# Performance work log

Measured on AMD Instinct MI355X. Metric: run time of the kernel, lower is better.

The kernel has to match this reference:

```python
import jax, jax.numpy as jnp
import numpy as np

OUT, IN, SPEC = 4096, 4096, 512


def _boundprop(last_uA, weight, bias, preact_lb, preact_ub, alpha):
    # simplex_coefficient: relu(W + b[:,None]) - relu(b[:,None]), shape [OUT, IN]
    simplex_coeff = jax.nn.relu(weight + bias[:, None]) - jax.nn.relu(bias[:, None])
    pos_uA = jnp.maximum(last_uA, 0.0)  # [1, SPEC, OUT]
    neg_uA = jnpum if False else jnp.minimum(last_uA, 0.0)

    # ---- simplex branch ----
    lb_u = preact_lb[..., None]  # [1, OUT, 1]
    ub_u = preact_ub[..., None]
    upper_coeff = jnp.where(ub_u <= 0, 0.0, jnp.where(lb_u >= 0, weight, simplex_coeff))  # [1,OUT,IN]
    upper_bias = jnp.where(preact_ub <= 0, 0.0,
                           jnp.where(preact_lb >= 0, bias, jnp.maximum(bias, 0.0)))  # [1,OUT]
    lower_d = (jnp.abs(preact_lb) >= jnp.abs(preact_ub)).astype(last_uA.dtype)  # [1,OUT]
    lower_coeff = jnp.where(ub_u <= 0, 0.0,
                            jnp.where(lb_u >= 0, weight, lower_d[..., None] * weight))  # [1,OUT,IN]
    lower_bias = jnp.where(preact_ub <= 0, 0.0,
                           jnp.where(preact_lb >= 0, bias, lower_d * bias))  # [1,OUT]
    one_minus_a = 1.0 - alpha              # [1,OUT,1]
    one_minus_a_s = 1.0 - alpha[..., 0]    # [1,OUT]
    upper_coeff = one_minus_a * upper_coeff
    lower_coeff = one_minus_a * lower_coeff
    upper_bias = one_minus_a_s * upper_bias
    lower_bias = one_minus_a_s * lower_bias
    simplex_uA = (jnp.einsum('bso,boi->bsi', pos_uA, upper_coeff)
                  + jnp.einsum('bso,boi->bsi', neg_uA, lower_coeff))  # [1,SPEC,IN]
    simplex_ubias = (jnp.einsum('bso,o->bs', pos_uA, upper_bias[0])
                     + jnp.einsum('bso,o->bs', neg_uA, lower_bias[0]))  # [1,SPEC]

    # ---- crown branch ----
    lb_r = jnp.minimum(preact_lb, 0.0)
    ub_r = jnp.maximum(preact_ub, 0.0)
    ub_r = jnp.maximum(ub_r, lb_r + 1e-8)
    upper_d = ub_r / (ub_r - lb_r)  # [1,OUT]
    upper_b = -lb_r * upper_d       # [1,OUT]
    ud = upper_d[:, None, :]        # [1,1,OUT]
    ld = (ud > 0.5).astype(last_uA.dtype)
    crown_uA_pre = ud * pos_uA + ld * neg_uA  # [1,SPEC,OUT]
    crown_ubias = jnp.einsum('bso,bo->bs', pos_uA, upper_b)  # [1,SPEC]
    w = alpha * weight              # [1,OUT,IN]
    b = alpha[..., 0] * bias        # [1,OUT]
    crown_uA = jnp.einsum('bso,boi->bsi', crown_uA_pre, w)   # [1,SPEC,IN]
    crown_ubias = crown_ubias + jnp.einsum('bso,o->bs', crown_uA_pre, b[0])

    return simplex_uA + crown_uA, simplex_ubias + crown_ubias


def setup_inputs() -> dict:
    key = jax.random.key(0)
    k1, k2, k3, k4, k5 = jax.random.split(key, 5)
    weight = jax.random.normal(k1, (OUT, IN), jnp.float32) * 0.02
    bias = jax.random.normal(k2, (OUT,), jnp.float32) * 0.02
    preact_lb = jax.random.normal(k3, (1, OUT), jnp.float32)
    # ensure ub > lb, with mixed-sign ranges so all relaxation branches are hit
    preact_ub = preact_lb + jnp.abs(jax.random.normal(k4, (1, OUT), jnp.float32)) + 1e-2
    last_uA = jax.random.normal(k5, (1, SPEC, OUT), jnp.float32)
    alpha = jnp.ones((1, OUT, 1), jnp.float32)
    return {'last_uA': last_uA, 'weight': weight, 'bias': bias,
            'preact_lb': preact_lb, 'preact_ub': preact_ub, 'alpha': alpha}


def reference(last_uA, weight, bias, preact_lb, preact_ub, alpha):
    uA, ubias = _boundprop(last_uA, weight, bias, preact_lb, preact_ub, alpha)
    return uA, ubias
```

## Files before the change

kernel.cpp:

```cpp
#include <hip/hip_runtime.h>
#include <hip/hip_bf16.h>
#include <stdint.h>

#define OUTN 4096
#define INN  4096
#define SPECN 512
#define BK 128
#define KT (OUTN / BK)

typedef __attribute__((ext_vector_type(8))) short short8;
typedef __attribute__((ext_vector_type(4))) float f32x4;

__device__ __forceinline__ ushort f2bf(float f) {
    uint32_t u = __float_as_uint(f);
    uint32_t r = (u + 0x7FFFu + ((u >> 16) & 1u)) >> 16;
    return (ushort)r;
}
__device__ __forceinline__ float bf2f(ushort u) {
    return __uint_as_float((uint32_t)u << 16);
}

__global__ __launch_bounds__(256) void prep(
    const float* __restrict__ uA, const float* __restrict__ W,
    const float* __restrict__ Bias, const float* __restrict__ Lb,
    const float* __restrict__ Ub, const float* __restrict__ Alpha,
    ushort* __restrict__ A1, ushort* __restrict__ A2, ushort* __restrict__ WT,
    unsigned long long* __restrict__ rowmask, float* __restrict__ ubias_out)
{
    const int tid = threadIdx.x;
    if (blockIdx.x < 512) {
        const int s = blockIdx.x;
        float acc = 0.f;
        unsigned long long msk = 0;
        for (int p = 0; p < 4; ++p) {
            const int o = p * 1024 + tid * 4;
            const float4 u4 = *(const float4*)&uA[(size_t)s * OUTN + o];
            const float4 lb4 = *(const float4*)&Lb[o];
            const float4 ub4 = *(const float4*)&Ub[o];
            const float4 b4 = *(const float4*)&Bias[o];
            const float4 a4 = *(const float4*)&Alpha[o];
            const float uu[4] = {u4.x, u4.y, u4.z, u4.w};
            const float lbv[4] = {lb4.x, lb4.y, lb4.z, lb4.w};
            const float ubv[4] = {ub4.x, ub4.y, ub4.z, ub4.w};
            const float bv[4] = {b4.x, b4.y, b4.z, b4.w};
            const float av[4] = {a4.x, a4.y, a4.z, a4.w};
            ushort r1[4], r2[4];
#pragma unroll
            for (int j = 0; j < 4; ++j) {
                const float u = uu[j], lb = lbv[j], ub = ubv[j], b = bv[j], a = av[j];
                const float pp = fmaxf(u, 0.f), nn = fminf(u, 0.f);
                const bool stneg = (ub <= 0.f);
                const bool stpos = (lb >= 0.f);
                const float lower_d = (fabsf(lb) >= fabsf(ub)) ? 1.f : 0.f;
                float lbr = fminf(lb, 0.f);
                float ubr = fmaxf(ub, 0.f);
                ubr = fmaxf(ubr, lbr + 1e-8f);
                const float ud = ubr / (ubr - lbr);
                const float upb = -lbr * ud;
                const float ldc = (ud > 0.5f) ? 1.f : 0.f;
                const float oma = 1.f - a;
                const float crown = ud * pp + ldc * nn;
                const float wcoef = a * crown +
                    oma * (stneg ? 0.f : (stpos ? (pp + nn) : lower_d * nn));
                const float scoef = (stneg || stpos) ? 0.f : oma * pp;
                const float ub_t = stneg ? 0.f : (stpos ? b : fmaxf(b, 0.f));
                const float lb_t = stneg ? 0.f : (stpos ? b : lower_d * b);
                acc += pp * (oma * ub_t + upb) + nn * (oma * lb_t) + crown * (a * b);
                r1[j] = f2bf(wcoef);
                r2[j] = f2bf(scoef);
            }
            *(ushort4*)&A1[(size_t)s * OUTN + o] = make_ushort4(r1[0], r1[1], r1[2], r1[3]);
            *(ushort4*)&A2[(size_t)s * OUTN + o] = make_ushort4(r2[0], r2[1], r2[2], r2[3]);
            if (((r2[0] | r2[1] | r2[2] | r2[3]) & 0x7FFF) != 0)
                msk |= 1ull << (p * 16 + (tid >> 4));
        }
#pragma unroll
        for (int off = 32; off; off >>= 1) {
            acc += __shfl_down(acc, off);
            msk |= __shfl_down(msk, off);
        }
        __shared__ float redf[4];
        __shared__ unsigned long long redm[4];
        if ((tid & 63) == 0) { redf[tid >> 6] = acc; redm[tid >> 6] = msk; }
        __syncthreads();
        if (tid == 0) {
            ubias_out[s] = redf[0] + redf[1] + redf[2] + redf[3];
            rowmask[s] = redm[0] | redm[1] | redm[2] | redm[3];
        }
    } else {
        __shared__ float t[64][65];
        const int tb = blockIdx.x - 512;
        const int bi = tb & 63, bo = tb >> 6;
        const int i0 = bi * 64, o0 = bo * 64;
        const int sub = tid >> 4;
        const int q4 = (tid & 15) * 4;
#pragma unroll
        for (int p = 0; p < 4; ++p) {
            const int ol = p * 16 + sub;
            const float4 w = *(const float4*)&W[(size_t)(o0 + ol) * INN + i0 + q4];
            t[q4 + 0][ol] = w.x;
            t[q4 + 1][ol] = w.y;
            t[q4 + 2][ol] = w.z;
            t[q4 + 3][ol] = w.w;
        }
        __syncthreads();
#pragma unroll
        for (int p = 0; p < 4; ++p) {
            const int il = p * 16 + sub;
            *(ushort4*)&WT[(size_t)(i0 + il) * OUTN + o0 + q4] =
                make_ushort4(f2bf(t[il][q4]), f2bf(t[il][q4 + 1]),
                             f2bf(t[il][q4 + 2]), f2bf(t[il][q4 + 3]));
        }
    }
}

__global__ __launch_bounds__(256) void gemm(
    const ushort* __restrict__ A1, const ushort* __restrict__ A2,
    const ushort* __restrict__ WT, const float* __restrict__ Bias,
    const unsigned long long* __restrict__ rowmask, float* __restrict__ outp)
{
    __shared__ __align__(16) ushort smem[2][2][64 * BK];

    const int bid = blockIdx.x;
    const int swz = (bid & 7) * 64 + (bid >> 3);
    const int bx = swz >> 3;
    const int by = swz & 7;
    const int i0 = bx * 64, s0 = by * 64;
    const int tid = threadIdx.x;
    const int lane = tid & 63;
    const int w = tid >> 6;

    unsigned long long smask = rowmask[s0 + lane];
#pragma unroll
    for (int off = 32; off; off >>= 1) smask |= __shfl_xor(smask, off);

    f32x4 acc[4][4] = {};

    auto stage = [&](int buf, int t) {
        const int ko = t * BK;
#pragma unroll
        for (int h = 0; h < 4; ++h) {
            const int c = w * 4 + h;
            const int row = c * 4 + (lane >> 4);
            const int g = (lane & 15) ^ (row & 15);
            __builtin_amdgcn_global_load_lds(
                (const __attribute__((address_space(1))) void*)(A1 + (size_t)(s0 + row) * OUTN + ko + g * 8),
                (__attribute__((address_space(3))) void*)&smem[0][buf][c * 512], 16, 0, 0);
            __builtin_amdgcn_global_load_lds(
                (const __attribute__((address_space(1))) void*)(WT + (size_t)(i0 + row) * OUTN + ko + g * 8),
                (__attribute__((address_space(3))) void*)&smem[1][buf][c * 512], 16, 0, 0);
        }
    };

    auto compute = [&](int buf) {
        const int kc = w * 4 + (lane >> 4);
        short8 av[4], bv[4];
#pragma unroll
        for (int m = 0; m < 4; ++m) {
            const int r = m * 16 + (lane & 15);
            av[m] = *(const short8*)&smem[0][buf][r * BK + (kc ^ (r & 15)) * 8];
        }
#pragma unroll
        for (int n = 0; n < 4; ++n) {
            const int r = n * 16 + (lane & 15);
            bv[n] = *(const short8*)&smem[1][buf][r * BK + (kc ^ (r & 15)) * 8];
        }
#pragma unroll
        for (int m = 0; m < 4; ++m)
#pragma unroll
            for (int n = 0; n < 4; ++n)
                acc[m][n] = __builtin_amdgcn_mfma_f32_16x16x32_bf16(
                    av[m], bv[n], acc[m][n], 0, 0, 0);
    };

    stage(0, 0);
    __syncthreads();
    for (int t = 0; t < KT - 1; ++t) {
        stage((t + 1) & 1, t + 1);
        compute(t & 1);
        __syncthreads();
    }
    compute((KT - 1) & 1);

    if (smask) {
        for (int b = 0; b < 64; ++b) {
            if (!((smask >> b) & 1)) continue;
            __syncthreads();
#pragma unroll
            for (int h = 0; h < 2; ++h) {
                const int c = w * 2 + h;
                const int row = c * 8 + (lane >> 3);
                const int g = (lane & 7) ^ (row & 7);
                __builtin_amdgcn_global_load_lds(
                    (const __attribute__((address_space(1))) void*)(A2 + (size_t)(s0 + row) * OUTN + b * 64 + g * 8),
                    (__attribute__((address_space(3))) void*)&smem[0][0][c * 512], 16, 0, 0);
                __builtin_amdgcn_global_load_lds(
                    (const __attribute__((address_space(1))) void*)(WT + (size_t)(i0 + row) * OUTN + b * 64 + g * 8),
                    (__attribute__((address_space(3))) void*)&smem[1][0][c * 512], 16, 0, 0);
            }
            __syncthreads();
            if (w < 2) {
                const int kk = w * 32;
                const int kc8 = (kk >> 3) + (lane >> 4);
                short8 av2[4], bw[4];
#pragma unroll
                for (int m = 0; m < 4; ++m) {
                    const int r = m * 16 + (lane & 15);
                    av2[m] = *(const short8*)&smem[0][0][r * 64 + (kc8 ^ (r & 7)) * 8];
                }
                const int kb = kk + (lane >> 4) * 8;
                const float4 b0 = *(const float4*)&Bias[b * 64 + kb];
                const float4 b1 = *(const float4*)&Bias[b * 64 + kb + 4];
                const float bb[8] = {b0.x, b0.y, b0.z, b0.w, b1.x, b1.y, b1.z, b1.w};
#pragma unroll
                for (int n = 0; n < 4; ++n) {
                    const int r = n * 16 + (lane & 15);
                    const short8 wv = *(const short8*)&smem[1][0][r * 64 + (kc8 ^ (r & 7)) * 8];
                    short8 sv;
#pragma unroll
                    for (int j = 0; j < 8; ++j) {
                        const float wf = bf2f((ushort)wv[j]);
                        sv[j] = (short)f2bf(fmaxf(wf + bb[j], 0.f) - fmaxf(bb[j], 0.f));
                    }
                    bw[n] = sv;
                }
#pragma unroll
                for (int m = 0; m < 4; ++m)
#pragma unroll
                    for (int n = 0; n < 4; ++n)
                        acc[m][n] = __builtin_amdgcn_mfma_f32_16x16x32_bf16(
                            av2[m], bw[n], acc[m][n], 0, 0, 0);
            }
        }
    }

    __syncthreads();
    float* facc = (float*)smem;
#pragma unroll
    for (int m = 0; m < 4; ++m)
#pragma unroll
        for (int n = 0; n < 4; ++n)
            *(f32x4*)&facc[w * 4096 + (m * 4 + n) * 256 + lane * 4] = acc[m][n];
    __syncthreads();
#pragma unroll
    for (int n = 0; n < 4; ++n) {
        f32x4 s = *(const f32x4*)&facc[(w * 4 + n) * 256 + lane * 4];
#pragma unroll
        for (int wp = 1; wp < 4; ++wp) {
            const f32x4 v = *(const f32x4*)&facc[wp * 4096 + (w * 4 + n) * 256 + lane * 4];
            s.x += v.x; s.y += v.y; s.z += v.z; s.w += v.w;
        }
        const int srow = s0 + w * 16 + (lane >> 4) * 4;
        const int icol = i0 + n * 16 + (lane & 15);
        outp[(size_t)(srow + 0) * INN + icol] = s.x;
        outp[(size_t)(srow + 1) * INN + icol] = s.y;
        outp[(size_t)(srow + 2) * INN + icol] = s.z;
        outp[(size_t)(srow + 3) * INN + icol] = s.w;
    }
}

extern "C" void kernel_launch(void* const* d_in, const int* in_sizes, int n_in,
                              void* d_out, int out_size, void* d_ws, size_t ws_size,
                              hipStream_t stream) {
    const float* uA    = (const float*)d_in[0];
    const float* W     = (const float*)d_in[1];
    const float* Bias  = (const float*)d_in[2];
    const float* Lb    = (const float*)d_in[3];
    const float* Ub    = (const float*)d_in[4];
    const float* Alpha = (const float*)d_in[5];
    float* outp = (float*)d_out;

    char* ws = (char*)d_ws;
    unsigned long long* rowmask = (unsigned long long*)ws;
    ushort* A1 = (ushort*)(ws + 4096);
    ushort* A2 = (ushort*)(ws + 4096 + (1u << 22));
    ushort* WT = (ushort*)(ws + 4096 + (2u << 22));

    prep<<<4608, 256, 0, stream>>>(uA, W, Bias, Lb, Ub, Alpha, A1, A2, WT,
                                   rowmask, outp + (size_t)SPECN * INN);
    gemm<<<512, 256, 0, stream>>>(A1, A2, WT, Bias, rowmask, outp);
}
```

Baseline: 145.5 us.

## Split GEMM K dimension in two, read A directly from global, add reduce kernel

Splits the K reduction of the GEMM across two blocks per output tile, doubling the grid to 1024 blocks. Each block writes a partial result to workspace and a new reduce kernel sums the two partials. The A operand and the simplex branch's A2/W tiles are now read straight from global memory into registers instead of being staged through LDS. This halves the LDS footprint and allows 4 blocks per CU. The aim is better occupancy and CU utilisation, at the cost of an extra kernel launch, an extra round trip of the partial outputs through memory, and uncoalesced global reads for A.

```diff
diff --git a/kernel.cpp b/kernel.cpp
--- a/kernel.cpp
+++ b/kernel.cpp
@@ -6,7 +6,9 @@
 #define INN  4096
 #define SPECN 512
 #define BK 128
-#define KT (OUTN / BK)
+#define KSPLIT 2
+#define KPB (OUTN / KSPLIT)
+#define TPB (KPB / BK)
 
 typedef __attribute__((ext_vector_type(8))) short short8;
 typedef __attribute__((ext_vector_type(4))) float f32x4;
@@ -114,18 +116,20 @@
     }
 }
 
-__global__ __launch_bounds__(256) void gemm(
+__global__ __launch_bounds__(256, 4) void gemm(
     const ushort* __restrict__ A1, const ushort* __restrict__ A2,
     const ushort* __restrict__ WT, const float* __restrict__ Bias,
-    const unsigned long long* __restrict__ rowmask, float* __restrict__ outp)
+    const unsigned long long* __restrict__ rowmask, float* __restrict__ P)
 {
-    __shared__ __align__(16) ushort smem[2][2][64 * BK];
+    __shared__ __align__(16) ushort sB[2][64 * BK];
 
     const int bid = blockIdx.x;
-    const int swz = (bid & 7) * 64 + (bid >> 3);
-    const int bx = swz >> 3;
-    const int by = swz & 7;
+    const int gid = (bid & 7) * 128 + (bid >> 3);
+    const int bx = gid >> 4;
+    const int by = (gid >> 1) & 7;
+    const int ks = gid & 1;
     const int i0 = bx * 64, s0 = by * 64;
+    const int k0 = ks * KPB;
     const int tid = threadIdx.x;
     const int lane = tid & 63;
     const int w = tid >> 6;
@@ -137,33 +141,30 @@
     f32x4 acc[4][4] = {};
 
     auto stage = [&](int buf, int t) {
-        const int ko = t * BK;
+        const int ko = k0 + t * BK;
 #pragma unroll
         for (int h = 0; h < 4; ++h) {
             const int c = w * 4 + h;
             const int row = c * 4 + (lane >> 4);
             const int g = (lane & 15) ^ (row & 15);
             __builtin_amdgcn_global_load_lds(
-                (const __attribute__((address_space(1))) void*)(A1 + (size_t)(s0 + row) * OUTN + ko + g * 8),
-                (__attribute__((address_space(3))) void*)&smem[0][buf][c * 512], 16, 0, 0);
-            __builtin_amdgcn_global_load_lds(
                 (const __attribute__((address_space(1))) void*)(WT + (size_t)(i0 + row) * OUTN + ko + g * 8),
-                (__attribute__((address_space(3))) void*)&smem[1][buf][c * 512], 16, 0, 0);
+                (__attribute__((address_space(3))) void*)&sB[buf][c * 512], 16, 0, 0);
         }
     };
 
-    auto compute = [&](int buf) {
+    auto compute = [&](int buf, int t) {
+        const int arow = lane & 15;
+        const int kb = k0 + t * BK + w * 32 + (lane >> 4) * 8;
+        short8 av[4], bv[4];
+#pragma unroll
+        for (int m = 0; m < 4; ++m)
+            av[m] = *(const short8*)&A1[(size_t)(s0 + m * 16 + arow) * OUTN + kb];
         const int kc = w * 4 + (lane >> 4);
-        short8 av[4], bv[4];
-#pragma unroll
-        for (int m = 0; m < 4; ++m) {
-            const int r = m * 16 + (lane & 15);
-            av[m] = *(const short8*)&smem[0][buf][r * BK + (kc ^ (r & 15)) * 8];
-        }
 #pragma unroll
         for (int n = 0; n < 4; ++n) {
-            const int r = n * 16 + (lane & 15);
-            bv[n] = *(const short8*)&smem[1][buf][r * BK + (kc ^ (r & 15)) * 8];
+            const int r = n * 16 + arow;
+            bv[n] = *(const short8*)&sB[buf][r * BK + (kc ^ (r & 15)) * 8];
         }
 #pragma unroll
         for (int m = 0; m < 4; ++m)
@@ -175,47 +176,29 @@
 
     stage(0, 0);
     __syncthreads();
-    for (int t = 0; t < KT - 1; ++t) {
-        stage((t + 1) & 1, t + 1);
-        compute(t & 1);
-        __syncthreads();
-    }
-    compute((KT - 1) & 1);
+    for (int t = 0; t < TPB; ++t) {
+        if (t + 1 < TPB) stage((t + 1) & 1, t + 1);
+        compute(t & 1, t);
+        if (t + 1 < TPB) __syncthreads();
+    }
 
     if (smask) {
-        for (int b = 0; b < 64; ++b) {
+        for (int b = ks * 32; b < ks * 32 + 32; ++b) {
             if (!((smask >> b) & 1)) continue;
-            __syncthreads();
-#pragma unroll
-            for (int h = 0; h < 2; ++h) {
-                const int c = w * 2 + h;
-                const int row = c * 8 + (lane >> 3);
-                const int g = (lane & 7) ^ (row & 7);
-                __builtin_amdgcn_global_load_lds(
-                    (const __attribute__((address_space(1))) void*)(A2 + (size_t)(s0 + row) * OUTN + b * 64 + g * 8),
-                    (__attribute__((address_space(3))) void*)&smem[0][0][c * 512], 16, 0, 0);
-                __builtin_amdgcn_global_load_lds(
-                    (const __attribute__((address_space(1))) void*)(WT + (size_t)(i0 + row) * OUTN + b * 64 + g * 8),
-                    (__attribute__((address_space(3))) void*)&smem[1][0][c * 512], 16, 0, 0);
-            }
-            __syncthreads();
             if (w < 2) {
                 const int kk = w * 32;
-                const int kc8 = (kk >> 3) + (lane >> 4);
+                const int arow = lane & 15;
+                const int kbb = b * 64 + kk + (lane >> 4) * 8;
                 short8 av2[4], bw[4];
 #pragma unroll
-                for (int m = 0; m < 4; ++m) {
-                    const int r = m * 16 + (lane & 15);
-                    av2[m] = *(const short8*)&smem[0][0][r * 64 + (kc8 ^ (r & 7)) * 8];
-                }
-                const int kb = kk + (lane >> 4) * 8;
-                const float4 b0 = *(const float4*)&Bias[b * 64 + kb];
-                const float4 b1 = *(const float4*)&Bias[b * 64 + kb + 4];
+                for (int m = 0; m < 4; ++m)
+                    av2[m] = *(const short8*)&A2[(size_t)(s0 + m * 16 + arow) * OUTN + kbb];
+                const float4 b0 = *(const float4*)&Bias[kbb];
+                const float4 b1 = *(const float4*)&Bias[kbb + 4];
                 const float bb[8] = {b0.x, b0.y, b0.z, b0.w, b1.x, b1.y, b1.z, b1.w};
 #pragma unroll
                 for (int n = 0; n < 4; ++n) {
-                    const int r = n * 16 + (lane & 15);
-                    const short8 wv = *(const short8*)&smem[1][0][r * 64 + (kc8 ^ (r & 7)) * 8];
+                    const short8 wv = *(const short8*)&WT[(size_t)(i0 + n * 16 + arow) * OUTN + kbb];
                     short8 sv;
 #pragma unroll
                     for (int j = 0; j < 8; ++j) {
@@ -235,28 +218,77 @@
     }
 
     __syncthreads();
-    float* facc = (float*)smem;
-#pragma unroll
-    for (int m = 0; m < 4; ++m)
-#pragma unroll
-        for (int n = 0; n < 4; ++n)
-            *(f32x4*)&facc[w * 4096 + (m * 4 + n) * 256 + lane * 4] = acc[m][n];
-    __syncthreads();
-#pragma unroll
-    for (int n = 0; n < 4; ++n) {
-        f32x4 s = *(const f32x4*)&facc[(w * 4 + n) * 256 + lane * 4];
-#pragma unroll
-        for (int wp = 1; wp < 4; ++wp) {
-            const f32x4 v = *(const f32x4*)&facc[wp * 4096 + (w * 4 + n) * 256 + lane * 4];
-            s.x += v.x; s.y += v.y; s.z += v.z; s.w += v.w;
-        }
-        const int srow = s0 + w * 16 + (lane >> 4) * 4;
-        const int icol = i0 + n * 16 + (lane & 15);
-        outp[(size_t)(srow + 0) * INN + icol] = s.x;
-        outp[(size_t)(srow + 1) * INN + icol] = s.y;
-        outp[(size_t)(srow + 2) * INN + icol] = s.z;
-        outp[(size_t)(srow + 3) * INN + icol] = s.w;
-    }
+    float* facc = (float*)&sB[0][0];
+    if (w >= 2) {
+#pragma unroll
+        for (int m = 0; m < 4; ++m)
+#pragma unroll
+            for (int n = 0; n < 4; ++n)
+                *(f32x4*)&facc[(w - 2) * 4096 + (m * 4 + n) * 256 + lane * 4] = acc[m][n];
+    }
+    __syncthreads();
+    if (w < 2) {
+#pragma unroll
+        for (int m = 0; m < 4; ++m)
+#pragma unroll
+            for (int n = 0; n < 4; ++n) {
+                const f32x4 v = *(const f32x4*)&facc[w * 4096 + (m * 4 + n) * 256 + lane * 4];
+                acc[m][n] += v;
+            }
+    }
+    __syncthreads();
+    if (w == 0) {
+#pragma unroll
+        for (int m = 2; m < 4; ++m)
+#pragma unroll
+            for (int n = 0; n < 4; ++n)
+                *(f32x4*)&facc[((m - 2) * 4 + n) * 256 + lane * 4] = acc[m][n];
+    } else if (w == 1) {
+#pragma unroll
+        for (int m = 0; m < 2; ++m)
+#pragma unroll
+            for (int n = 0; n < 4; ++n)
+                *(f32x4*)&facc[2048 + (m * 4 + n) * 256 + lane * 4] = acc[m][n];
+    }
+    __syncthreads();
+    float* Pp = P + (size_t)ks * SPECN * INN;
+    if (w == 0) {
+#pragma unroll
+        for (int m = 0; m < 2; ++m)
+#pragma unroll
+            for (int n = 0; n < 4; ++n) {
+                const f32x4 v = *(const f32x4*)&facc[2048 + (m * 4 + n) * 256 + lane * 4];
+                f32x4 s = acc[m][n]; s += v;
+                const int srow = s0 + m * 16 + (lane >> 4) * 4;
+                const int icol = i0 + n * 16 + (lane & 15);
+#pragma unroll
+                for (int r = 0; r < 4; ++r)
+                    Pp[(size_t)(srow + r) * INN + icol] = s[r];
+            }
+    } else if (w == 1) {
+#pragma unroll
+        for (int m = 2; m < 4; ++m)
+#pragma unroll
+            for (int n = 0; n < 4; ++n) {
+                const f32x4 v = *(const f32x4*)&facc[((m - 2) * 4 + n) * 256 + lane * 4];
+                f32x4 s = acc[m][n]; s += v;
+                const int srow = s0 + m * 16 + (lane >> 4) * 4;
+                const int icol = i0 + n * 16 + (lane & 15);
+#pragma unroll
+                for (int r = 0; r < 4; ++r)
+                    Pp[(size_t)(srow + r) * INN + icol] = s[r];
+            }
+    }
+}
+
+__global__ __launch_bounds__(256) void reduce(
+    const float* __restrict__ P, float* __restrict__ outp)
+{
+    const size_t idx = ((size_t)blockIdx.x * 256 + threadIdx.x) * 4;
+    const f32x4 a = *(const f32x4*)&P[idx];
+    const f32x4 b = *(const f32x4*)&P[(size_t)SPECN * INN + idx];
+    f32x4 s = a; s += b;
+    *(f32x4*)&outp[idx] = s;
 }
 
 extern "C" void kernel_launch(void* const* d_in, const int* in_sizes, int n_in,
@@ -275,8 +307,10 @@
     ushort* A1 = (ushort*)(ws + 4096);
     ushort* A2 = (ushort*)(ws + 4096 + (1u << 22));
     ushort* WT = (ushort*)(ws + 4096 + (2u << 22));
+    float*  P  = (float*)(ws + 4096 + (2u << 22) + (1u << 25));
 
     prep<<<4608, 256, 0, stream>>>(uA, W, Bias, Lb, Ub, Alpha, A1, A2, WT,
                                    rowmask, outp + (size_t)SPECN * INN);
-    gemm<<<512, 256, 0, stream>>>(A1, A2, WT, Bias, rowmask, outp);
-}
+    gemm<<<1024, 256, 0, stream>>>(A1, A2, WT, Bias, rowmask, P);
+    reduce<<<(SPECN * INN) / 1024, 256, 0, stream>>>(P, outp);
+}
```

Measured after the change: 167.5 us. 1.15x slower.
